# Kernel optimization log

Hardware: AMD Instinct MI355X
Metric: run time of the kernel (lower is better)

Reference implementation:

```python
import jax, jax.numpy as jnp
import numpy as np

WS = 8
HEADS = 12


def _dwconv(x, w, b):
    # x: (N, C, H, W); w: (C, 1, 3, 3) depthwise, zero pad 1
    y = jax.lax.conv_general_dilated(
        x, w, window_strides=(1, 1), padding=((1, 1), (1, 1)),
        dimension_numbers=("NCHW", "OIHW", "NCHW"), feature_group_count=x.shape[1])
    return y + b[None, :, None, None]


def _sepconv(x, dw, db, pw, pb):
    y = _dwconv(x, dw, db)
    # pointwise 1x1 conv: (N,C,H,W) x (O,C) -> (N,O,H,W)
    return jnp.einsum("nchw,oc->nohw", y, pw) + pb[None, :, None, None]


def _rel_pos_index(ws):
    coords = np.stack(np.meshgrid(np.arange(ws), np.arange(ws), indexing="ij"))  # (2, ws, ws)
    cf = coords.reshape(2, -1)
    rel = cf[:, :, None] - cf[:, None, :]          # (2, ws*ws, ws*ws)
    rel = rel.transpose(1, 2, 0).copy()
    rel[..., 0] += ws - 1
    rel[..., 1] += ws - 1
    rel[..., 0] *= 2 * ws - 1
    return rel.sum(-1)                             # (ws*ws, ws*ws)


def setup_inputs() -> dict:
    key = jax.random.key(0)
    ks = jax.random.split(key, 16)
    B, T, C, H, W = 2, 1, 384, 192, 192
    s = 0.02
    inp = {
        "vid": jax.random.normal(ks[0], (B, T, C, H, W), jnp.float32),
        "qd_w": jax.random.normal(ks[1], (C, 1, 3, 3), jnp.float32) * s,
        "qd_b": jnp.zeros((C,), jnp.float32),
        "qp_w": jax.random.normal(ks[2], (C, C), jnp.float32) * s,
        "qp_b": jnp.zeros((C,), jnp.float32),
        "kd_w": jax.random.normal(ks[3], (C, 1, 3, 3), jnp.float32) * s,
        "kd_b": jnp.zeros((C,), jnp.float32),
        "kp_w": jax.random.normal(ks[4], (C, C), jnp.float32) * s,
        "kp_b": jnp.zeros((C,), jnp.float32),
        "vd_w": jax.random.normal(ks[5], (C, 1, 3, 3), jnp.float32) * s,
        "vd_b": jnp.zeros((C,), jnp.float32),
        "vp_w": jax.random.normal(ks[6], (C, C), jnp.float32) * s,
        "vp_b": jnp.zeros((C,), jnp.float32),
        "rpb_table": jax.random.normal(ks[7], ((2 * WS - 1) ** 2, HEADS), jnp.float32) * s,
        "proj_w": jax.random.normal(ks[8], (C, C), jnp.float32) * s,
        "proj_b": jnp.zeros((C,), jnp.float32),
    }
    return inp


def reference(vid, qd_w, qd_b, qp_w, qp_b, kd_w, kd_b, kp_w, kp_b,
              vd_w, vd_b, vp_w, vp_b, rpb_table, proj_w, proj_b):
    B, T, C, H, W = vid.shape
    heads, ws = HEADS, WS
    hd = C // heads
    scale = hd ** -0.5
    x = vid.reshape(B * T, C, H, W)

    q = _sepconv(x, qd_w, qd_b, qp_w, qp_b) * scale
    k = _sepconv(x, kd_w, kd_b, kp_w, kp_b)
    v = _sepconv(x, vd_w, vd_b, vp_w, vp_b)

    nh, nw = H // ws, W // ws

    def win(z):  # (N, C, H, W) -> (N*nh*nw, heads, ws*ws, hd)
        N = z.shape[0]
        z = z.reshape(N, heads, hd, nh, ws, nw, ws)
        z = z.transpose(0, 3, 5, 1, 4, 6, 2)  # N, nh, nw, heads, ws, ws, hd
        return z.reshape(N * nh * nw, heads, ws * ws, hd)

    qw, kw, vw = win(q), win(k), win(v)

    # product search within window (dists = q . k), rel-pos bias softmax
    attn = jnp.einsum("nhqd,nhkd->nhqk", qw, kw)
    rp_idx = _rel_pos_index(ws)  # static (64, 64)
    bias = rpb_table[rp_idx.reshape(-1)].reshape(ws * ws, ws * ws, heads)
    bias = bias.transpose(2, 0, 1)  # (heads, 64, 64)
    attn = jax.nn.softmax(attn + bias[None], axis=-1)

    # weighted patch sum (ps=1 -> pixels)
    out = jnp.einsum("nhqk,nhkd->nhqd", attn, vw)  # (N*nh*nw, heads, ws*ws, hd)

    # un-window, merge heads into (h c) channel order, then token projection
    out = out.reshape(B * T, nh, nw, heads, ws, ws, hd)
    out = out.transpose(0, 1, 4, 2, 5, 3, 6).reshape(B * T, H, W, heads * hd)
    out = out @ proj_w.T + proj_b

    # fold (ps=1, stride0=1): identity overlap-add, zvid == 1
    out = out.transpose(0, 3, 1, 2).reshape(B, T, C, H, W)
    return out
```

## Files before the change

kernel.cpp:

```cpp
#include <hip/hip_runtime.h>

#define CCH 384
#define HH 192
#define WWD 192
#define NIMG 2
#define HWP (HH * WWD)
#define PTOT (NIMG * HWP)
#define HEADS 12
#define HD 32
#define NWIN 24
#define WINS 576
#define EELEM ((size_t)NIMG * CCH * HWP)
#define WMAT 147456

typedef __attribute__((ext_vector_type(8))) short bh8;
typedef __attribute__((ext_vector_type(8))) unsigned short us8;
typedef __attribute__((ext_vector_type(4))) unsigned short us4;
typedef __attribute__((ext_vector_type(4))) float fx4;

__device__ __forceinline__ unsigned short f2bf(float f) {
    unsigned u = __float_as_uint(f);
    u += 0x7fffu + ((u >> 16) & 1u);
    return (unsigned short)(u >> 16);
}

__global__ __launch_bounds__(256) void wcvt(
    const float* __restrict__ a, const float* __restrict__ b,
    const float* __restrict__ c, const float* __restrict__ d,
    unsigned short* __restrict__ o)
{
    int idx8 = (blockIdx.x * 256 + threadIdx.x) * 8;
    int which = idx8 / WMAT;
    int loc = idx8 - which * WMAT;
    const float* s = (which == 0) ? a : (which == 1) ? b : (which == 2) ? c : d;
    float4 v0 = *(const float4*)(s + loc);
    float4 v1 = *(const float4*)(s + loc + 4);
    us8 ov;
    ov[0] = f2bf(v0.x); ov[1] = f2bf(v0.y); ov[2] = f2bf(v0.z); ov[3] = f2bf(v0.w);
    ov[4] = f2bf(v1.x); ov[5] = f2bf(v1.y); ov[6] = f2bf(v1.z); ov[7] = f2bf(v1.w);
    *(us8*)(o + idx8) = ov;
}

__global__ __launch_bounds__(256) void dwgather(
    const float* __restrict__ x,
    const float* __restrict__ qw, const float* __restrict__ qb,
    const float* __restrict__ kw, const float* __restrict__ kb,
    const float* __restrict__ vw, const float* __restrict__ vb,
    unsigned short* __restrict__ oq, unsigned short* __restrict__ ok,
    unsigned short* __restrict__ ov)
{
    __shared__ float halo[64 * 121];

    int bid = blockIdx.x;
    int b = (bid & 7) * 864 + (bid >> 3);
    int wtx  = b % 24;
    int strip = b / 24;
    int chv  = strip % 6;
    int nwy  = strip / 6;
    int wy   = nwy % 24;
    int n    = nwy / 24;

    int h0 = wy * 8, w0 = wtx * 8;
    int tid = threadIdx.x;
    int c   = tid & 63;
    int pxg = tid >> 6;
    int cg  = chv * 64 + c;
    int widx = n * WINS + wy * NWIN + wtx;

    const float* xbase = x + (size_t)n * CCH * HWP + (size_t)(chv * 64) * HWP;

    for (int j = tid; j < 1920; j += 256) {
        int seg = j % 3;
        int t   = j / 3;
        int rr  = t % 10;
        int cc  = t / 10;
        int hr  = h0 - 1 + rr;
        int cb  = w0 - 2 + seg * 4;
        float4 val = make_float4(0.f, 0.f, 0.f, 0.f);
        if (hr >= 0 && hr < HH) {
            const float* p = xbase + (size_t)cc * HWP + (size_t)hr * WWD;
            if (cb >= 0 && cb + 4 <= WWD) {
                val = *(const float4*)(p + cb);
            } else {
                if (cb + 0 >= 0 && cb + 0 < WWD) val.x = p[cb + 0];
                if (cb + 1 >= 0 && cb + 1 < WWD) val.y = p[cb + 1];
                if (cb + 2 >= 0 && cb + 2 < WWD) val.z = p[cb + 2];
                if (cb + 3 >= 0 && cb + 3 < WWD) val.w = p[cb + 3];
            }
        }
        int hb = cc * 121 + rr * 12 + seg * 4;
        halo[hb + 0] = val.x;
        halo[hb + 1] = val.y;
        halo[hb + 2] = val.z;
        halo[hb + 3] = val.w;
    }

    float wq[9], wk[9], wv[9];
#pragma unroll
    for (int t = 0; t < 9; ++t) {
        wq[t] = qw[cg * 9 + t];
        wk[t] = kw[cg * 9 + t];
        wv[t] = vw[cg * 9 + t];
    }
    float bqv = qb[cg], bkv = kb[cg], bvv = vb[cg];

    __syncthreads();

#pragma unroll
    for (int i = 0; i < 16; ++i) {
        int px = pxg * 16 + i;
        int pr = px >> 3, pc = px & 7;
        float sq = 0.f, sk = 0.f, sv = 0.f;
#pragma unroll
        for (int dr = 0; dr < 3; ++dr)
#pragma unroll
            for (int dc = 0; dc < 3; ++dc) {
                float xv = halo[c * 121 + (pr + dr) * 12 + pc + dc + 1];
                int t = dr * 3 + dc;
                sq = fmaf(xv, wq[t], sq);
                sk = fmaf(xv, wk[t], sk);
                sv = fmaf(xv, wv[t], sv);
            }
        size_t ob = ((size_t)widx * 64 + px) * CCH + cg;
        oq[ob] = f2bf(sq + bqv);
        ok[ob] = f2bf(sk + bkv);
        ov[ob] = f2bf(sv + bvv);
    }
}

template<int ORIENT>
__global__ __launch_bounds__(256) void pw_gemm(
    const unsigned short* __restrict__ Y, const unsigned short* __restrict__ Wb,
    const float* __restrict__ bias, float scale,
    unsigned short* __restrict__ outb, float* __restrict__ outf)
{
    __shared__ unsigned short Wt[128][40];
    __shared__ unsigned short Yt[128][40];

    int tid = threadIdx.x;
    int pp0 = blockIdx.x * 128;
    int cm0 = blockIdx.y * 128;
    int lid = tid & 63, wid = tid >> 6;
    int wr = wid >> 1, wc = wid & 1;
    int li = lid & 15, g = lid >> 4;
    int srow = tid >> 2;
    int skoff = (tid & 3) * 8;

    fx4 acc[4][4];
#pragma unroll
    for (int i = 0; i < 4; ++i)
#pragma unroll
        for (int j = 0; j < 4; ++j) acc[i][j] = (fx4){0.f, 0.f, 0.f, 0.f};

    const unsigned short* WpG = Wb + (size_t)(cm0 + srow) * CCH + skoff;
    const unsigned short* YpG = Y  + (size_t)(pp0 + srow) * CCH + skoff;
    bh8 w0 = *(const bh8*)(WpG);
    bh8 w1 = *(const bh8*)(WpG + (size_t)64 * CCH);
    bh8 y0 = *(const bh8*)(YpG);
    bh8 y1 = *(const bh8*)(YpG + (size_t)64 * CCH);

    typedef unsigned short (*tile_t)[40];
    tile_t Asrc = (ORIENT == 1) ? Wt : Yt;
    tile_t Bsrc = (ORIENT == 1) ? Yt : Wt;

    for (int kt = 0; kt < 12; ++kt) {
        __syncthreads();
        *(bh8*)&Wt[srow][skoff]      = w0;
        *(bh8*)&Wt[64 + srow][skoff] = w1;
        *(bh8*)&Yt[srow][skoff]      = y0;
        *(bh8*)&Yt[64 + srow][skoff] = y1;
        __syncthreads();
        if (kt < 11) {
            int ko = (kt + 1) * 32;
            w0 = *(const bh8*)(WpG + ko);
            w1 = *(const bh8*)(WpG + ko + (size_t)64 * CCH);
            y0 = *(const bh8*)(YpG + ko);
            y1 = *(const bh8*)(YpG + ko + (size_t)64 * CCH);
        }
        bh8 a[4], b[4];
#pragma unroll
        for (int mf = 0; mf < 4; ++mf)
            a[mf] = *(const bh8*)&Asrc[wr * 64 + mf * 16 + li][g * 8];
#pragma unroll
        for (int nf = 0; nf < 4; ++nf)
            b[nf] = *(const bh8*)&Bsrc[wc * 64 + nf * 16 + li][g * 8];
#pragma unroll
        for (int mf = 0; mf < 4; ++mf)
#pragma unroll
            for (int nf = 0; nf < 4; ++nf)
                acc[mf][nf] = __builtin_amdgcn_mfma_f32_16x16x32_bf16(
                    a[mf], b[nf], acc[mf][nf], 0, 0, 0);
    }

    if (ORIENT == 1) {
#pragma unroll
        for (int mf = 0; mf < 4; ++mf) {
            int c = cm0 + wr * 64 + mf * 16 + g * 4;
            float4 bv = *(const float4*)&bias[c];
#pragma unroll
            for (int nf = 0; nf < 4; ++nf) {
                int p = pp0 + wc * 64 + nf * 16 + li;
                us4 o;
                o[0] = f2bf((acc[mf][nf][0] + bv.x) * scale);
                o[1] = f2bf((acc[mf][nf][1] + bv.y) * scale);
                o[2] = f2bf((acc[mf][nf][2] + bv.z) * scale);
                o[3] = f2bf((acc[mf][nf][3] + bv.w) * scale);
                *(us4*)(outb + (size_t)p * CCH + c) = o;
            }
        }
    } else if (ORIENT == 2) {
#pragma unroll
        for (int nf = 0; nf < 4; ++nf) {
            int c = cm0 + wc * 64 + nf * 16 + li;
            float bv = bias[c];
#pragma unroll
            for (int mf = 0; mf < 4; ++mf) {
                int p = pp0 + wr * 64 + mf * 16 + g * 4;
                int n = p / HWP;
                int pl = p - n * HWP;
                us4 o;
                o[0] = f2bf(acc[mf][nf][0] + bv);
                o[1] = f2bf(acc[mf][nf][1] + bv);
                o[2] = f2bf(acc[mf][nf][2] + bv);
                o[3] = f2bf(acc[mf][nf][3] + bv);
                *(us4*)(outb + (size_t)(n * CCH + c) * HWP + pl) = o;
            }
        }
    } else {
#pragma unroll
        for (int nf = 0; nf < 4; ++nf) {
            int c = cm0 + wc * 64 + nf * 16 + li;
            float bv = bias[c];
#pragma unroll
            for (int mf = 0; mf < 4; ++mf) {
                int p = pp0 + wr * 64 + mf * 16 + g * 4;
                int n = p / HWP;
                int rem = p - n * HWP;
                int win = rem >> 6, t = rem & 63;
                int h = (win / NWIN) * 8 + (t >> 3);
                int w = (win % NWIN) * 8 + (t & 7);
                float4 o;
                o.x = acc[mf][nf][0] + bv;
                o.y = acc[mf][nf][1] + bv;
                o.z = acc[mf][nf][2] + bv;
                o.w = acc[mf][nf][3] + bv;
                *(float4*)(outf + (size_t)(n * CCH + c) * HWP + h * WWD + w) = o;
            }
        }
    }
}

__global__ __launch_bounds__(256) void attn(
    const unsigned short* __restrict__ q, const unsigned short* __restrict__ k,
    const unsigned short* __restrict__ v, const float* __restrict__ rpb,
    unsigned short* __restrict__ o)
{
    __shared__ float rpbs[225 * HEADS];
    __shared__ unsigned short Pl[4][64][72];

    int tid = threadIdx.x, lid = tid & 63, wid = tid >> 6;
    int wl = blockIdx.x;
    int n = wl / WINS, winl = wl - n * WINS;
    int li = lid & 15, g = lid >> 4;

    for (int i = tid; i < 225 * HEADS; i += 256) rpbs[i] = rpb[i];
    __syncthreads();

    const fx4 z = (fx4){0.f, 0.f, 0.f, 0.f};

    for (int hq = wid; hq < HEADS; hq += 4) {
        const unsigned short* qp = q + (size_t)(wl * 64) * CCH + hq * HD + g * 8;
        const unsigned short* kp = k + (size_t)(wl * 64) * CCH + hq * HD + g * 8;
        bh8 aq[4], bk[4];
#pragma unroll
        for (int mf = 0; mf < 4; ++mf)
            aq[mf] = *(const bh8*)(qp + (size_t)(mf * 16 + li) * CCH);
#pragma unroll
        for (int nf = 0; nf < 4; ++nf)
            bk[nf] = *(const bh8*)(kp + (size_t)(nf * 16 + li) * CCH);

        fx4 s[4][4];
#pragma unroll
        for (int mf = 0; mf < 4; ++mf)
#pragma unroll
            for (int nf = 0; nf < 4; ++nf)
                s[mf][nf] = __builtin_amdgcn_mfma_f32_16x16x32_bf16(aq[mf], bk[nf], z, 0, 0, 0);

#pragma unroll
        for (int mf = 0; mf < 4; ++mf)
#pragma unroll
            for (int nf = 0; nf < 4; ++nf)
#pragma unroll
                for (int r = 0; r < 4; ++r) {
                    int tq = mf * 16 + g * 4 + r, tk = nf * 16 + li;
                    int dy = (tq >> 3) - (tk >> 3) + 7;
                    int dx = (tq & 7) - (tk & 7) + 7;
                    s[mf][nf][r] += rpbs[(dy * 15 + dx) * HEADS + hq];
                }

        float inv_[4][4];
#pragma unroll
        for (int mf = 0; mf < 4; ++mf)
#pragma unroll
            for (int r = 0; r < 4; ++r) {
                float m = s[mf][0][r];
#pragma unroll
                for (int nf = 1; nf < 4; ++nf) m = fmaxf(m, s[mf][nf][r]);
                m = fmaxf(m, __shfl_xor(m, 1));
                m = fmaxf(m, __shfl_xor(m, 2));
                m = fmaxf(m, __shfl_xor(m, 4));
                m = fmaxf(m, __shfl_xor(m, 8));
                float sum = 0.f;
#pragma unroll
                for (int nf = 0; nf < 4; ++nf) {
                    float e = __expf(s[mf][nf][r] - m);
                    s[mf][nf][r] = e;
                    sum += e;
                }
                sum += __shfl_xor(sum, 1);
                sum += __shfl_xor(sum, 2);
                sum += __shfl_xor(sum, 4);
                sum += __shfl_xor(sum, 8);
                inv_[mf][r] = 1.f / sum;
            }

#pragma unroll
        for (int mf = 0; mf < 4; ++mf)
#pragma unroll
            for (int nf = 0; nf < 4; ++nf)
#pragma unroll
                for (int r = 0; r < 4; ++r)
                    Pl[wid][mf * 16 + g * 4 + r][nf * 16 + li] =
                        f2bf(s[mf][nf][r] * inv_[mf][r]);

        fx4 o2[2][4];
#pragma unroll
        for (int m2 = 0; m2 < 2; ++m2)
#pragma unroll
            for (int nf = 0; nf < 4; ++nf) o2[m2][nf] = z;
#pragma unroll
        for (int ks = 0; ks < 2; ++ks) {
            bh8 av[2], bp[4];
#pragma unroll
            for (int m2 = 0; m2 < 2; ++m2)
                av[m2] = *(const bh8*)(v + (size_t)(n * CCH + hq * HD + m2 * 16 + li) * HWP
                                         + winl * 64 + ks * 32 + g * 8);
#pragma unroll
            for (int nf = 0; nf < 4; ++nf)
                bp[nf] = *(const bh8*)&Pl[wid][nf * 16 + li][ks * 32 + g * 8];
#pragma unroll
            for (int m2 = 0; m2 < 2; ++m2)
#pragma unroll
                for (int nf = 0; nf < 4; ++nf)
                    o2[m2][nf] = __builtin_amdgcn_mfma_f32_16x16x32_bf16(
                        av[m2], bp[nf], o2[m2][nf], 0, 0, 0);
        }
#pragma unroll
        for (int nf = 0; nf < 4; ++nf) {
            int tq = nf * 16 + li;
#pragma unroll
            for (int m2 = 0; m2 < 2; ++m2) {
                int d = hq * HD + m2 * 16 + g * 4;
                us4 ov;
                ov[0] = f2bf(o2[m2][nf][0]);
                ov[1] = f2bf(o2[m2][nf][1]);
                ov[2] = f2bf(o2[m2][nf][2]);
                ov[3] = f2bf(o2[m2][nf][3]);
                *(us4*)(o + (size_t)(wl * 64 + tq) * CCH + d) = ov;
            }
        }
    }
}

extern "C" void kernel_launch(void* const* d_in, const int* in_sizes, int n_in,
                              void* d_out, int out_size, void* d_ws, size_t ws_size,
                              hipStream_t stream) {
    const float* vid  = (const float*)d_in[0];
    const float* qd_w = (const float*)d_in[1];
    const float* qd_b = (const float*)d_in[2];
    const float* qp_w = (const float*)d_in[3];
    const float* qp_b = (const float*)d_in[4];
    const float* kd_w = (const float*)d_in[5];
    const float* kd_b = (const float*)d_in[6];
    const float* kp_w = (const float*)d_in[7];
    const float* kp_b = (const float*)d_in[8];
    const float* vd_w = (const float*)d_in[9];
    const float* vd_b = (const float*)d_in[10];
    const float* vp_w = (const float*)d_in[11];
    const float* vp_b = (const float*)d_in[12];
    const float* rpb  = (const float*)d_in[13];
    const float* pj_w = (const float*)d_in[14];
    const float* pj_b = (const float*)d_in[15];

    unsigned short* ws16 = (unsigned short*)d_ws;
    unsigned short* tr0 = ws16 + 3 * EELEM;
    unsigned short* tr1 = ws16 + 4 * EELEM;
    unsigned short* tr2 = ws16 + 5 * EELEM;
    unsigned short* Wb  = ws16 + 6 * EELEM;
    unsigned short* qb  = ws16;
    unsigned short* kb  = ws16 + EELEM;
    unsigned short* vb  = ws16 + 2 * EELEM;
    unsigned short* ob  = tr0;

    wcvt<<<288, 256, 0, stream>>>(qp_w, kp_w, vp_w, pj_w, Wb);
    dwgather<<<NIMG * WINS * 6, 256, 0, stream>>>(
        vid, qd_w, qd_b, kd_w, kd_b, vd_w, vd_b, tr0, tr1, tr2);

    dim3 gg(PTOT / 128, 3);
    const float scale = 0.17677669529663687f;
    pw_gemm<1><<<gg, 256, 0, stream>>>(tr0, Wb,             qp_b, scale, qb, nullptr);
    pw_gemm<1><<<gg, 256, 0, stream>>>(tr1, Wb + WMAT,      kp_b, 1.0f,  kb, nullptr);
    pw_gemm<2><<<gg, 256, 0, stream>>>(tr2, Wb + 2 * WMAT,  vp_b, 1.0f,  vb, nullptr);

    attn<<<NIMG * WINS, 256, 0, stream>>>(qb, kb, vb, rpb, ob);

    pw_gemm<3><<<gg, 256, 0, stream>>>(ob, Wb + 3 * WMAT, pj_b, 1.0f, nullptr, (float*)d_out);
}
```

Before: 405.4 us.

## Load GEMM tiles directly to LDS and halve depthwise channel strip width

```diff
diff --git a/kernel.cpp b/kernel.cpp
--- a/kernel.cpp
+++ b/kernel.cpp
@@ -22,6 +22,12 @@
     unsigned u = __float_as_uint(f);
     u += 0x7fffu + ((u >> 16) & 1u);
     return (unsigned short)(u >> 16);
+}
+
+__device__ __forceinline__ void gload16(const void* g, void* l) {
+    __builtin_amdgcn_global_load_lds(
+        (const __attribute__((address_space(1))) void*)g,
+        (__attribute__((address_space(3))) void*)l, 16, 0, 0);
 }
 
 __global__ __launch_bounds__(256) void wcvt(
@@ -49,27 +55,27 @@
     unsigned short* __restrict__ oq, unsigned short* __restrict__ ok,
     unsigned short* __restrict__ ov)
 {
-    __shared__ float halo[64 * 121];
+    __shared__ float halo[32 * 121];
 
     int bid = blockIdx.x;
-    int b = (bid & 7) * 864 + (bid >> 3);
-    int wtx  = b % 24;
-    int strip = b / 24;
-    int chv  = strip % 6;
-    int nwy  = strip / 6;
-    int wy   = nwy % 24;
-    int n    = nwy / 24;
+    int b = (bid & 7) * 1728 + (bid >> 3);
+    int wtx   = b % 24;
+    int rest  = b / 24;
+    int chv   = rest % 12;
+    int nwy   = rest / 12;
+    int wy    = nwy % 24;
+    int n     = nwy / 24;
 
     int h0 = wy * 8, w0 = wtx * 8;
     int tid = threadIdx.x;
-    int c   = tid & 63;
-    int pxg = tid >> 6;
-    int cg  = chv * 64 + c;
+    int c   = tid & 31;
+    int pxg = tid >> 5;
+    int cg  = chv * 32 + c;
     int widx = n * WINS + wy * NWIN + wtx;
 
-    const float* xbase = x + (size_t)n * CCH * HWP + (size_t)(chv * 64) * HWP;
-
-    for (int j = tid; j < 1920; j += 256) {
+    const float* xbase = x + (size_t)n * CCH * HWP + (size_t)(chv * 32) * HWP;
+
+    for (int j = tid; j < 960; j += 256) {
         int seg = j % 3;
         int t   = j / 3;
         int rr  = t % 10;
@@ -107,21 +113,19 @@
     __syncthreads();
 
 #pragma unroll
-    for (int i = 0; i < 16; ++i) {
-        int px = pxg * 16 + i;
-        int pr = px >> 3, pc = px & 7;
+    for (int i = 0; i < 8; ++i) {
         float sq = 0.f, sk = 0.f, sv = 0.f;
 #pragma unroll
         for (int dr = 0; dr < 3; ++dr)
 #pragma unroll
             for (int dc = 0; dc < 3; ++dc) {
-                float xv = halo[c * 121 + (pr + dr) * 12 + pc + dc + 1];
+                float xv = halo[c * 121 + (pxg + dr) * 12 + i + dc + 1];
                 int t = dr * 3 + dc;
                 sq = fmaf(xv, wq[t], sq);
                 sk = fmaf(xv, wk[t], sk);
                 sv = fmaf(xv, wv[t], sv);
             }
-        size_t ob = ((size_t)widx * 64 + px) * CCH + cg;
+        size_t ob = ((size_t)widx * 64 + pxg * 8 + i) * CCH + cg;
         oq[ob] = f2bf(sq + bqv);
         ok[ob] = f2bf(sk + bkv);
         ov[ob] = f2bf(sv + bvv);
@@ -134,8 +138,8 @@
     const float* __restrict__ bias, float scale,
     unsigned short* __restrict__ outb, float* __restrict__ outf)
 {
-    __shared__ unsigned short Wt[128][40];
-    __shared__ unsigned short Yt[128][40];
+    __shared__ unsigned short Wt[128][32];
+    __shared__ unsigned short Yt[128][32];
 
     int tid = threadIdx.x;
     int pp0 = blockIdx.x * 128;
@@ -143,8 +147,9 @@
     int lid = tid & 63, wid = tid >> 6;
     int wr = wid >> 1, wc = wid & 1;
     int li = lid & 15, g = lid >> 4;
-    int srow = tid >> 2;
-    int skoff = (tid & 3) * 8;
+
+    int srow = (lid >> 2);
+    int scol = (lid & 3) * 8;
 
     fx4 acc[4][4];
 #pragma unroll
@@ -152,31 +157,23 @@
 #pragma unroll
         for (int j = 0; j < 4; ++j) acc[i][j] = (fx4){0.f, 0.f, 0.f, 0.f};
 
-    const unsigned short* WpG = Wb + (size_t)(cm0 + srow) * CCH + skoff;
-    const unsigned short* YpG = Y  + (size_t)(pp0 + srow) * CCH + skoff;
-    bh8 w0 = *(const bh8*)(WpG);
-    bh8 w1 = *(const bh8*)(WpG + (size_t)64 * CCH);
-    bh8 y0 = *(const bh8*)(YpG);
-    bh8 y1 = *(const bh8*)(YpG + (size_t)64 * CCH);
-
-    typedef unsigned short (*tile_t)[40];
+    typedef unsigned short (*tile_t)[32];
     tile_t Asrc = (ORIENT == 1) ? Wt : Yt;
     tile_t Bsrc = (ORIENT == 1) ? Yt : Wt;
 
+    const unsigned short* Wg0 = Wb + (size_t)(cm0 + wid * 32 + srow) * CCH + scol;
+    const unsigned short* Yg0 = Y  + (size_t)(pp0 + wid * 32 + srow) * CCH + scol;
+
     for (int kt = 0; kt < 12; ++kt) {
+        int k0 = kt * 32;
         __syncthreads();
-        *(bh8*)&Wt[srow][skoff]      = w0;
-        *(bh8*)&Wt[64 + srow][skoff] = w1;
-        *(bh8*)&Yt[srow][skoff]      = y0;
-        *(bh8*)&Yt[64 + srow][skoff] = y1;
+#pragma unroll
+        for (int qi = 0; qi < 2; ++qi) {
+            gload16(Wg0 + (size_t)qi * 16 * CCH + k0, &Wt[wid * 32 + qi * 16][0]);
+            gload16(Yg0 + (size_t)qi * 16 * CCH + k0, &Yt[wid * 32 + qi * 16][0]);
+        }
         __syncthreads();
-        if (kt < 11) {
-            int ko = (kt + 1) * 32;
-            w0 = *(const bh8*)(WpG + ko);
-            w1 = *(const bh8*)(WpG + ko + (size_t)64 * CCH);
-            y0 = *(const bh8*)(YpG + ko);
-            y1 = *(const bh8*)(YpG + ko + (size_t)64 * CCH);
-        }
+
         bh8 a[4], b[4];
 #pragma unroll
         for (int mf = 0; mf < 4; ++mf)
@@ -403,7 +400,7 @@
     unsigned short* ob  = tr0;
 
     wcvt<<<288, 256, 0, stream>>>(qp_w, kp_w, vp_w, pj_w, Wb);
-    dwgather<<<NIMG * WINS * 6, 256, 0, stream>>>(
+    dwgather<<<NIMG * WINS * 12, 256, 0, stream>>>(
         vid, qd_w, qd_b, kd_w, kd_b, vd_w, vd_b, tr0, tr1, tr2);
 
     dim3 gg(PTOT / 128, 3);
```

New measurement: 436.5 us. 1.08x slower.

## Double-buffer pointwise GEMM tiles via direct global-to-LDS loads; transpose depthwise weights

Applied to the files above, without the earlier changes.

```diff
diff --git a/kernel.cpp b/kernel.cpp
--- a/kernel.cpp
+++ b/kernel.cpp
@@ -22,6 +22,12 @@
     unsigned u = __float_as_uint(f);
     u += 0x7fffu + ((u >> 16) & 1u);
     return (unsigned short)(u >> 16);
+}
+
+__device__ __forceinline__ void gload16(const void* g, void* l) {
+    __builtin_amdgcn_global_load_lds(
+        (const __attribute__((address_space(1))) void*)g,
+        (__attribute__((address_space(3))) void*)l, 16, 0, 0);
 }
 
 __global__ __launch_bounds__(256) void wcvt(
@@ -41,11 +47,25 @@
     *(us8*)(o + idx8) = ov;
 }
 
+__global__ __launch_bounds__(256) void wprep(
+    const float* __restrict__ q, const float* __restrict__ k,
+    const float* __restrict__ v, float* __restrict__ o)
+{
+    int idx = blockIdx.x * 256 + threadIdx.x;
+    if (idx >= 3 * 9 * CCH) return;
+    int ten = idx / (9 * CCH);
+    int rem = idx - ten * (9 * CCH);
+    int tap = rem / CCH;
+    int c   = rem - tap * CCH;
+    const float* s = (ten == 0) ? q : (ten == 1) ? k : v;
+    o[idx] = s[c * 9 + tap];
+}
+
 __global__ __launch_bounds__(256) void dwgather(
     const float* __restrict__ x,
-    const float* __restrict__ qw, const float* __restrict__ qb,
-    const float* __restrict__ kw, const float* __restrict__ kb,
-    const float* __restrict__ vw, const float* __restrict__ vb,
+    const float* __restrict__ wt,
+    const float* __restrict__ qb, const float* __restrict__ kb,
+    const float* __restrict__ vb,
     unsigned short* __restrict__ oq, unsigned short* __restrict__ ok,
     unsigned short* __restrict__ ov)
 {
@@ -98,9 +118,9 @@
     float wq[9], wk[9], wv[9];
 #pragma unroll
     for (int t = 0; t < 9; ++t) {
-        wq[t] = qw[cg * 9 + t];
-        wk[t] = kw[cg * 9 + t];
-        wv[t] = vw[cg * 9 + t];
+        wq[t] = wt[t * CCH + cg];
+        wk[t] = wt[9 * CCH + t * CCH + cg];
+        wv[t] = wt[18 * CCH + t * CCH + cg];
     }
     float bqv = qb[cg], bkv = kb[cg], bvv = vb[cg];
 
@@ -134,8 +154,8 @@
     const float* __restrict__ bias, float scale,
     unsigned short* __restrict__ outb, float* __restrict__ outf)
 {
-    __shared__ unsigned short Wt[128][40];
-    __shared__ unsigned short Yt[128][40];
+    __shared__ unsigned short Wt[2][128][32];
+    __shared__ unsigned short Yt[2][128][32];
 
     int tid = threadIdx.x;
     int pp0 = blockIdx.x * 128;
@@ -143,8 +163,9 @@
     int lid = tid & 63, wid = tid >> 6;
     int wr = wid >> 1, wc = wid & 1;
     int li = lid & 15, g = lid >> 4;
-    int srow = tid >> 2;
-    int skoff = (tid & 3) * 8;
+
+    int srow = (lid >> 2);
+    int scol = (lid & 3) * 8;
 
     fx4 acc[4][4];
 #pragma unroll
@@ -152,44 +173,46 @@
 #pragma unroll
         for (int j = 0; j < 4; ++j) acc[i][j] = (fx4){0.f, 0.f, 0.f, 0.f};
 
-    const unsigned short* WpG = Wb + (size_t)(cm0 + srow) * CCH + skoff;
-    const unsigned short* YpG = Y  + (size_t)(pp0 + srow) * CCH + skoff;
-    bh8 w0 = *(const bh8*)(WpG);
-    bh8 w1 = *(const bh8*)(WpG + (size_t)64 * CCH);
-    bh8 y0 = *(const bh8*)(YpG);
-    bh8 y1 = *(const bh8*)(YpG + (size_t)64 * CCH);
-
-    typedef unsigned short (*tile_t)[40];
-    tile_t Asrc = (ORIENT == 1) ? Wt : Yt;
-    tile_t Bsrc = (ORIENT == 1) ? Yt : Wt;
+    typedef unsigned short (*tile3)[128][32];
+    tile3 A3 = (ORIENT == 1) ? Wt : Yt;
+    tile3 B3 = (ORIENT == 1) ? Yt : Wt;
+
+    const unsigned short* Wg0 = Wb + (size_t)(cm0 + wid * 32 + srow) * CCH + scol;
+    const unsigned short* Yg0 = Y  + (size_t)(pp0 + wid * 32 + srow) * CCH + scol;
+
+#pragma unroll
+    for (int qi = 0; qi < 2; ++qi) {
+        gload16(Wg0 + (size_t)qi * 16 * CCH, &Wt[0][wid * 32 + qi * 16][0]);
+        gload16(Yg0 + (size_t)qi * 16 * CCH, &Yt[0][wid * 32 + qi * 16][0]);
+    }
+    __syncthreads();
 
     for (int kt = 0; kt < 12; ++kt) {
-        __syncthreads();
-        *(bh8*)&Wt[srow][skoff]      = w0;
-        *(bh8*)&Wt[64 + srow][skoff] = w1;
-        *(bh8*)&Yt[srow][skoff]      = y0;
-        *(bh8*)&Yt[64 + srow][skoff] = y1;
-        __syncthreads();
+        int cur = kt & 1;
         if (kt < 11) {
-            int ko = (kt + 1) * 32;
-            w0 = *(const bh8*)(WpG + ko);
-            w1 = *(const bh8*)(WpG + ko + (size_t)64 * CCH);
-            y0 = *(const bh8*)(YpG + ko);
-            y1 = *(const bh8*)(YpG + ko + (size_t)64 * CCH);
-        }
+            int k1 = (kt + 1) * 32;
+#pragma unroll
+            for (int qi = 0; qi < 2; ++qi) {
+                gload16(Wg0 + (size_t)qi * 16 * CCH + k1, &Wt[cur ^ 1][wid * 32 + qi * 16][0]);
+                gload16(Yg0 + (size_t)qi * 16 * CCH + k1, &Yt[cur ^ 1][wid * 32 + qi * 16][0]);
+            }
+        }
+
         bh8 a[4], b[4];
 #pragma unroll
         for (int mf = 0; mf < 4; ++mf)
-            a[mf] = *(const bh8*)&Asrc[wr * 64 + mf * 16 + li][g * 8];
+            a[mf] = *(const bh8*)&A3[cur][wr * 64 + mf * 16 + li][g * 8];
 #pragma unroll
         for (int nf = 0; nf < 4; ++nf)
-            b[nf] = *(const bh8*)&Bsrc[wc * 64 + nf * 16 + li][g * 8];
+            b[nf] = *(const bh8*)&B3[cur][wc * 64 + nf * 16 + li][g * 8];
 #pragma unroll
         for (int mf = 0; mf < 4; ++mf)
 #pragma unroll
             for (int nf = 0; nf < 4; ++nf)
                 acc[mf][nf] = __builtin_amdgcn_mfma_f32_16x16x32_bf16(
                     a[mf], b[nf], acc[mf][nf], 0, 0, 0);
+
+        __syncthreads();
     }
 
     if (ORIENT == 1) {
@@ -397,14 +420,16 @@
     unsigned short* tr1 = ws16 + 4 * EELEM;
     unsigned short* tr2 = ws16 + 5 * EELEM;
     unsigned short* Wb  = ws16 + 6 * EELEM;
+    float* dwT          = (float*)(Wb + 4 * WMAT);
     unsigned short* qb  = ws16;
     unsigned short* kb  = ws16 + EELEM;
     unsigned short* vb  = ws16 + 2 * EELEM;
     unsigned short* ob  = tr0;
 
     wcvt<<<288, 256, 0, stream>>>(qp_w, kp_w, vp_w, pj_w, Wb);
+    wprep<<<41, 256, 0, stream>>>(qd_w, kd_w, vd_w, dwT);
     dwgather<<<NIMG * WINS * 6, 256, 0, stream>>>(
-        vid, qd_w, qd_b, kd_w, kd_b, vd_w, vd_b, tr0, tr1, tr2);
+        vid, dwT, qd_b, kd_b, vd_b, tr0, tr1, tr2);
 
     dim3 gg(PTOT / 128, 3);
     const float scale = 0.17677669529663687f;
```

Measured after the change: 413.4 us. No clear change (+2.0%).
